# Kernel optimization log

Hardware: AMD Instinct MI355X
Metric: run time of the kernel (lower is better)

The kernel has to match this reference:

```python
import jax, jax.numpy as jnp
import numpy as np

B = 1024
HP_ORDER = 4
N_GRID = 72 * (8 ** HP_ORDER)  # 294912 rotations in the SO(3) healpix grid


def _random_rotmats(key, n):
    """Uniform random rotation matrices via normalized quaternions."""
    q = jax.random.normal(key, (n, 4), dtype=jnp.float32)
    q = q / jnp.linalg.norm(q, axis=-1, keepdims=True)
    w, x, y, z = q[:, 0], q[:, 1], q[:, 2], q[:, 3]
    R = jnp.stack([
        jnp.stack([1 - 2 * (y * y + z * z), 2 * (x * y - w * z), 2 * (x * z + w * y)], axis=-1),
        jnp.stack([2 * (x * y + w * z), 1 - 2 * (x * x + z * z), 2 * (y * z - w * x)], axis=-1),
        jnp.stack([2 * (x * z - w * y), 2 * (y * z + w * x), 1 - 2 * (x * x + y * y)], axis=-1),
    ], axis=-2)  # [n, 3, 3]
    return R


def setup_inputs() -> dict:
    key = jax.random.key(0)
    k1, k2 = jax.random.split(key)
    rotMat = _random_rotmats(k1, B)            # [B, 3, 3] query rotations
    output_rotmats = _random_rotmats(k2, N_GRID)  # [N, 3, 3] fixed grid (buffer)
    return {"rotMat": rotMat, "output_rotmats": output_rotmats}


def reference(rotMat, output_rotmats):
    # trace(A @ R_n^T) == sum_ij A_ij * R_n_ij  -> GEMM with K=9
    sim = jnp.einsum('bij,nij->bn', rotMat, output_rotmats)  # [B, N]
    idxs = jnp.argmax(sim, axis=1)                            # [B]
    dot_trace = jnp.max(sim, axis=1)                          # [B]
    nearest = output_rotmats[idxs]                            # [B, 3, 3]
    return dot_trace, nearest
```

## Files before the change

### kernel.cpp

```cpp
#include <hip/hip_runtime.h>

#define B_TOTAL 1024
#define NGRID   294912
#define NTILES  (NGRID / 16)
#define MARGIN  6e-4f
#define CAP     (1u << 20)

#define QBLK    256
#define QTILES  (QBLK / 16)
#define NSLICE  512
#define TPB     (NTILES / NSLICE)
#define TPW2    (TPB / 4)

#define KEYS_OFF   0u
#define WSMAX_OFF  8192u
#define CNT_OFF    12288u
#define CAND_OFF   16384u
#define APACK_OFF  4210688u
#define GPACK_OFF  4276224u
#define WS_NEED    23150592u

typedef __attribute__((ext_vector_type(8))) short short8v;
typedef __attribute__((ext_vector_type(4))) float float4v;

__device__ __forceinline__ unsigned short f2bf(float x) {
    unsigned u = __float_as_uint(x);
    unsigned r = ((u >> 16) & 1u) + 0x7FFFu;
    return (unsigned short)((u + r) >> 16);
}
__device__ __forceinline__ float bf2f(unsigned short b) {
    return __uint_as_float(((unsigned)b) << 16);
}
__device__ __forceinline__ unsigned ford(float f) {
    unsigned u = __float_as_uint(f);
    return (u & 0x80000000u) ? ~u : (u | 0x80000000u);
}
__device__ __forceinline__ float funord(unsigned u) {
    return __uint_as_float((u & 0x80000000u) ? (u & 0x7FFFFFFFu) : ~u);
}

__global__ __launch_bounds__(256)
void so3_init_kernel(unsigned long long* __restrict__ keys,
                     unsigned* __restrict__ wsmax, unsigned* __restrict__ cnt) {
    int i = blockIdx.x * 256 + threadIdx.x;
    if (i < B_TOTAL) { keys[i] = 0ull; wsmax[i] = 0u; }
    if (i == 0) *cnt = 0u;
}

__global__ __launch_bounds__(256)
void so3_pack_kernel(const float* __restrict__ src, unsigned* __restrict__ dst,
                     int nrows, int isA) {
    int id = blockIdx.x * 256 + threadIdx.x;
    if (id >= nrows * 16) return;
    int r = id >> 4, i = id & 15;
    unsigned w = 0;
    #pragma unroll
    for (int h = 0; h < 2; ++h) {
        int s = i * 2 + h;
        unsigned short v = 0;
        if (s < 27) {
            int k = (s < 9) ? s : (s < 18 ? s - 9 : s - 18);
            float x = src[(size_t)r * 9 + k];
            unsigned short hi = f2bf(x);
            int wantLo = isA ? (s >= 18) : (s >= 9 && s < 18);
            v = wantLo ? f2bf(x - bf2f(hi)) : hi;
        }
        w |= ((unsigned)v) << (16 * h);
    }
    dst[id] = w;
}

__device__ __forceinline__ void stage_A(const unsigned short* __restrict__ Ap,
                                        unsigned short* sB, int t, int qbase) {
    #pragma unroll
    for (int i = 0; i < QBLK / 64; ++i) {
        int id = t + i * 256;
        int row = id >> 2, kb = id & 3;
        uint4 v = *(const uint4*)(Ap + (size_t)(qbase + row) * 32 + kb * 8);
        int skb = kb ^ ((row >> 1) & 3);
        *(uint4*)((char*)sB + row * 64 + skb * 16) = v;
    }
}

__device__ __forceinline__ float tree_max9(const float* m4) {
    float a = fmaxf(fmaxf(m4[0], m4[1]), m4[2]);
    float b = fmaxf(fmaxf(m4[3], m4[4]), m4[5]);
    float c = fmaxf(fmaxf(m4[6], m4[7]), m4[8]);
    return fmaxf(fmaxf(a, b), c);
}

__global__ __launch_bounds__(256, 4)
void so3_mfma_max_kernel(const unsigned short* __restrict__ Ap,
                         const unsigned short* __restrict__ Gp,
                         unsigned* __restrict__ wsmax) {
    __shared__ __align__(16) unsigned short sB[QBLK * 32];
    __shared__ float sW[4][QTILES][4][16];
    const int t = threadIdx.x, l = t & 63, w = t >> 6;
    const int lr = l & 15, lk = l >> 4;
    const int qbase = blockIdx.y * QBLK;

    stage_A(Ap, sB, t, qbase);

    const int tile0 = blockIdx.x * TPB + w * TPW2;
    short8v af[TPW2];
    #pragma unroll
    for (int i = 0; i < TPW2; ++i)
        af[i] = *(const short8v*)(Gp + (size_t)((tile0 + i) * 16 + lr) * 32 + lk * 8);

    __syncthreads();

    for (int qt = 0; qt < QTILES; ++qt) {
        const int row = qt * 16 + lr;
        const int skb = lk ^ ((row >> 1) & 3);
        short8v bf = *(const short8v*)((const char*)sB + row * 64 + skb * 16);
        float m4[TPW2];
        #pragma unroll
        for (int i = 0; i < TPW2; ++i) {
            float4v c = {0.f, 0.f, 0.f, 0.f};
            c = __builtin_amdgcn_mfma_f32_16x16x32_bf16(af[i], bf, c, 0, 0, 0);
            m4[i] = fmaxf(fmaxf(c[0], c[1]), fmaxf(c[2], c[3]));
        }
        sW[w][qt][lk][lr] = tree_max9(m4);
    }
    __syncthreads();

    {
        int e = t;
        int qt = e >> 4, q = e & 15;
        float v = -1e30f;
        #pragma unroll
        for (int ww = 0; ww < 4; ++ww)
            #pragma unroll
            for (int kk = 0; kk < 4; ++kk)
                v = fmaxf(v, sW[ww][qt][kk][q]);
        unsigned u = ford(v);
        unsigned* p = wsmax + qbase + e;
        if (u > *p) atomicMax(p, u);
    }
}

__global__ __launch_bounds__(256, 4)
void so3_mfma_cand_kernel(const unsigned short* __restrict__ Ap,
                          const unsigned short* __restrict__ Gp,
                          const unsigned* __restrict__ wsmax,
                          unsigned* __restrict__ cnt,
                          unsigned* __restrict__ cands) {
    __shared__ __align__(16) unsigned short sB[QBLK * 32];
    __shared__ float sThr[QBLK];
    const int t = threadIdx.x, l = t & 63, w = t >> 6;
    const int lr = l & 15, lk = l >> 4;
    const int qbase = blockIdx.y * QBLK;

    stage_A(Ap, sB, t, qbase);
    sThr[t] = funord(wsmax[qbase + t]) - MARGIN;

    const int tile0 = blockIdx.x * TPB + w * TPW2;
    short8v af[TPW2];
    #pragma unroll
    for (int i = 0; i < TPW2; ++i)
        af[i] = *(const short8v*)(Gp + (size_t)((tile0 + i) * 16 + lr) * 32 + lk * 8);

    __syncthreads();

    for (int qt = 0; qt < QTILES; ++qt) {
        const int row = qt * 16 + lr;
        const float thr = sThr[row];
        const int skb = lk ^ ((row >> 1) & 3);
        short8v bf = *(const short8v*)((const char*)sB + row * 64 + skb * 16);
        #pragma unroll
        for (int i = 0; i < TPW2; ++i) {
            float4v c = {0.f, 0.f, 0.f, 0.f};
            c = __builtin_amdgcn_mfma_f32_16x16x32_bf16(af[i], bf, c, 0, 0, 0);
            float m4 = fmaxf(fmaxf(c[0], c[1]), fmaxf(c[2], c[3]));
            if (m4 >= thr) {
                int b = qbase + row;
                #pragma unroll
                for (int r = 0; r < 4; ++r) {
                    if (c[r] >= thr) {
                        int n = (tile0 + i) * 16 + lk * 4 + r;
                        unsigned idx = atomicAdd(cnt, 1u);
                        if (idx < CAP)
                            cands[idx] = ((unsigned)b << 19) | (unsigned)n;
                    }
                }
            }
        }
    }
}

__global__ __launch_bounds__(256)
void so3_rescore_kernel(const float* __restrict__ A, const float* __restrict__ G,
                        const unsigned* __restrict__ cnt,
                        const unsigned* __restrict__ cands,
                        unsigned long long* __restrict__ keys) {
    unsigned total = *cnt;
    if (total > CAP) total = CAP;
    const unsigned stride = gridDim.x * 256;
    for (unsigned i = blockIdx.x * 256 + threadIdx.x; i < total; i += stride) {
        unsigned cd = cands[i];
        int b = (int)(cd >> 19), n = (int)(cd & 0x7FFFFu);
        const float* a = A + (size_t)b * 9;
        const float* g = G + (size_t)n * 9;
        float d;
        d = a[0] * g[0];
        d = fmaf(a[1], g[1], d);
        d = fmaf(a[2], g[2], d);
        d = fmaf(a[3], g[3], d);
        d = fmaf(a[4], g[4], d);
        d = fmaf(a[5], g[5], d);
        d = fmaf(a[6], g[6], d);
        d = fmaf(a[7], g[7], d);
        d = fmaf(a[8], g[8], d);
        unsigned long long key =
            ((unsigned long long)ford(d) << 32) | (unsigned)(~n);
        unsigned long long seen = keys[b];
        if (key > seen) atomicMax(&keys[b], key);
    }
}

__global__ __launch_bounds__(256)
void so3_final_kernel(const float* __restrict__ G,
                      const unsigned long long* __restrict__ keys,
                      float* __restrict__ out) {
    int b = blockIdx.x * 256 + threadIdx.x;
    if (b >= B_TOTAL) return;
    unsigned long long key = keys[b];
    unsigned hi = (unsigned)(key >> 32);
    int idx = (int)(~(unsigned)key);
    out[b] = funord(hi);
    const float* g = G + (size_t)idx * 9;
    float* o = out + B_TOTAL + (size_t)b * 9;
    #pragma unroll
    for (int k = 0; k < 9; ++k) o[k] = g[k];
}

#define FB_NBLK  2048
#define FB_CHUNK (NGRID / FB_NBLK)
#define FB_NTHR  128
#define FB_BPT   8
__global__ __launch_bounds__(FB_NTHR, 4)
void so3_fb_partial_kernel(const float* __restrict__ A, const float* __restrict__ G,
                           unsigned long long* __restrict__ ws) {
    __shared__ __align__(16) float sG[FB_CHUNK * 12];
    const int t = threadIdx.x;
    const int n0 = blockIdx.x * FB_CHUNK;
    for (int i = t; i < FB_CHUNK * 9; i += FB_NTHR) {
        int row = i / 9, k = i - row * 9;
        sG[row * 12 + k] = G[(size_t)n0 * 9 + i];
    }
    float a[FB_BPT][9];
    #pragma unroll
    for (int j = 0; j < FB_BPT; ++j) {
        const float* ap = A + (size_t)(j * FB_NTHR + t) * 9;
        #pragma unroll
        for (int k = 0; k < 9; ++k) a[j][k] = ap[k];
    }
    float best[FB_BPT]; int bidx[FB_BPT];
    #pragma unroll
    for (int j = 0; j < FB_BPT; ++j) { best[j] = -1e30f; bidx[j] = 0; }
    __syncthreads();
    #pragma unroll 2
    for (int n = 0; n < FB_CHUNK; ++n) {
        const float4* gv = (const float4*)(sG + n * 12);
        const float4 gA = gv[0], gB = gv[1];
        const float g8 = sG[n * 12 + 8];
        const int vn = n0 + n;
        #pragma unroll
        for (int j = 0; j < FB_BPT; ++j) {
            float d;
            d = a[j][0] * gA.x; d = fmaf(a[j][1], gA.y, d); d = fmaf(a[j][2], gA.z, d);
            d = fmaf(a[j][3], gA.w, d); d = fmaf(a[j][4], gB.x, d); d = fmaf(a[j][5], gB.y, d);
            d = fmaf(a[j][6], gB.z, d); d = fmaf(a[j][7], gB.w, d); d = fmaf(a[j][8], g8, d);
            if (d > best[j]) { best[j] = d; bidx[j] = vn; }
        }
    }
    #pragma unroll
    for (int j = 0; j < FB_BPT; ++j) {
        unsigned long long key =
            ((unsigned long long)ford(best[j]) << 32) | (unsigned)(~bidx[j]);
        unsigned long long seen = ws[j * FB_NTHR + t];
        if (key > seen) atomicMax(&ws[j * FB_NTHR + t], key);
    }
}

extern "C" void kernel_launch(void* const* d_in, const int* in_sizes, int n_in,
                              void* d_out, int out_size, void* d_ws, size_t ws_size,
                              hipStream_t stream) {
    const float* A = (const float*)d_in[0];
    const float* G = (const float*)d_in[1];
    float* out = (float*)d_out;
    char* ws = (char*)d_ws;
    unsigned long long* keys = (unsigned long long*)(ws + KEYS_OFF);
    unsigned* wsmax = (unsigned*)(ws + WSMAX_OFF);
    unsigned* cnt   = (unsigned*)(ws + CNT_OFF);
    unsigned* cands = (unsigned*)(ws + CAND_OFF);
    unsigned short* Ap = (unsigned short*)(ws + APACK_OFF);
    unsigned short* Gp = (unsigned short*)(ws + GPACK_OFF);

    if (ws_size < WS_NEED) {
        hipLaunchKernelGGL(so3_init_kernel, dim3(4), dim3(256), 0, stream,
                           keys, wsmax, cnt);
        hipLaunchKernelGGL(so3_fb_partial_kernel, dim3(FB_NBLK), dim3(FB_NTHR),
                           0, stream, A, G, keys);
        hipLaunchKernelGGL(so3_final_kernel, dim3(4), dim3(256), 0, stream,
                           G, keys, out);
        return;
    }

    hipLaunchKernelGGL(so3_init_kernel, dim3(4), dim3(256), 0, stream,
                       keys, wsmax, cnt);
    hipLaunchKernelGGL(so3_pack_kernel, dim3((B_TOTAL * 16) / 256), dim3(256),
                       0, stream, A, (unsigned*)Ap, B_TOTAL, 1);
    hipLaunchKernelGGL(so3_pack_kernel, dim3((NGRID * 16) / 256), dim3(256),
                       0, stream, G, (unsigned*)Gp, NGRID, 0);
    hipLaunchKernelGGL(so3_mfma_max_kernel, dim3(NSLICE, B_TOTAL / QBLK),
                       dim3(256), 0, stream, Ap, Gp, wsmax);
    hipLaunchKernelGGL(so3_mfma_cand_kernel, dim3(NSLICE, B_TOTAL / QBLK),
                       dim3(256), 0, stream, Ap, Gp, wsmax, cnt, cands);
    hipLaunchKernelGGL(so3_rescore_kernel, dim3(128), dim3(256), 0, stream,
                       A, G, cnt, cands, keys);
    hipLaunchKernelGGL(so3_final_kernel, dim3(4), dim3(256), 0, stream,
                       G, keys, out);
}
```

Measured before the change: 87.90 us.

## Fuse max and candidate passes into one kernel with block-local threshold

Merges the max-reduction and candidate-collection kernels into a single kernel that computes a per-block query max, then filters candidates against that local threshold. Candidates are buffered in shared memory and flushed with one global atomic per block, and the slice count is halved so each wave handles more tiles. This removes a launch, the global max round-trip and per-candidate global atomics. The trade-off is that the local threshold is looser, so more candidates reach rescoring and the CAP overflow risk grows.

New measurement: 147.5 us. 67.7% more time.

```diff
diff --git a/kernel.cpp b/kernel.cpp
--- a/kernel.cpp
+++ b/kernel.cpp
@@ -8,12 +8,12 @@
 
 #define QBLK    256
 #define QTILES  (QBLK / 16)
-#define NSLICE  512
+#define NSLICE  256
 #define TPB     (NTILES / NSLICE)
-#define TPW2    (TPB / 4)
+#define TPW     (TPB / 4)
+#define SCAP    4096
 
 #define KEYS_OFF   0u
-#define WSMAX_OFF  8192u
 #define CNT_OFF    12288u
 #define CAND_OFF   16384u
 #define APACK_OFF  4210688u
@@ -41,9 +41,9 @@
 
 __global__ __launch_bounds__(256)
 void so3_init_kernel(unsigned long long* __restrict__ keys,
-                     unsigned* __restrict__ wsmax, unsigned* __restrict__ cnt) {
+                     unsigned* __restrict__ cnt) {
     int i = blockIdx.x * 256 + threadIdx.x;
-    if (i < B_TOTAL) { keys[i] = 0ull; wsmax[i] = 0u; }
+    if (i < B_TOTAL) keys[i] = 0ull;
     if (i == 0) *cnt = 0u;
 }
 
@@ -82,110 +82,98 @@
     }
 }
 
-__device__ __forceinline__ float tree_max9(const float* m4) {
-    float a = fmaxf(fmaxf(m4[0], m4[1]), m4[2]);
-    float b = fmaxf(fmaxf(m4[3], m4[4]), m4[5]);
-    float c = fmaxf(fmaxf(m4[6], m4[7]), m4[8]);
-    return fmaxf(fmaxf(a, b), c);
-}
-
 __global__ __launch_bounds__(256, 4)
-void so3_mfma_max_kernel(const unsigned short* __restrict__ Ap,
-                         const unsigned short* __restrict__ Gp,
-                         unsigned* __restrict__ wsmax) {
+void so3_fused_kernel(const unsigned short* __restrict__ Ap,
+                      const unsigned short* __restrict__ Gp,
+                      unsigned* __restrict__ cnt,
+                      unsigned* __restrict__ cands) {
     __shared__ __align__(16) unsigned short sB[QBLK * 32];
     __shared__ float sW[4][QTILES][4][16];
+    __shared__ float sThr[QBLK];
+    __shared__ unsigned sCand[SCAP];
+    __shared__ unsigned sCnt, sBase;
+
     const int t = threadIdx.x, l = t & 63, w = t >> 6;
     const int lr = l & 15, lk = l >> 4;
     const int qbase = blockIdx.y * QBLK;
 
     stage_A(Ap, sB, t, qbase);
-
-    const int tile0 = blockIdx.x * TPB + w * TPW2;
-    short8v af[TPW2];
-    #pragma unroll
-    for (int i = 0; i < TPW2; ++i)
+    if (t == 0) sCnt = 0;
+
+    const int tile0 = blockIdx.x * TPB + w * TPW;
+    short8v af[TPW];
+    #pragma unroll
+    for (int i = 0; i < TPW; ++i)
         af[i] = *(const short8v*)(Gp + (size_t)((tile0 + i) * 16 + lr) * 32 + lk * 8);
 
     __syncthreads();
 
+    #pragma unroll 2
     for (int qt = 0; qt < QTILES; ++qt) {
         const int row = qt * 16 + lr;
         const int skb = lk ^ ((row >> 1) & 3);
         short8v bf = *(const short8v*)((const char*)sB + row * 64 + skb * 16);
-        float m4[TPW2];
-        #pragma unroll
-        for (int i = 0; i < TPW2; ++i) {
+        float m = -1e30f;
+        #pragma unroll
+        for (int i = 0; i < TPW; ++i) {
             float4v c = {0.f, 0.f, 0.f, 0.f};
             c = __builtin_amdgcn_mfma_f32_16x16x32_bf16(af[i], bf, c, 0, 0, 0);
-            m4[i] = fmaxf(fmaxf(c[0], c[1]), fmaxf(c[2], c[3]));
+            float m3 = fmaxf(fmaxf(c[0], c[1]), c[2]);
+            m = fmaxf(fmaxf(m3, c[3]), m);
         }
-        sW[w][qt][lk][lr] = tree_max9(m4);
+        sW[w][qt][lk][lr] = m;
     }
     __syncthreads();
 
     {
-        int e = t;
-        int qt = e >> 4, q = e & 15;
+        int qt = t >> 4, q = t & 15;
         float v = -1e30f;
         #pragma unroll
         for (int ww = 0; ww < 4; ++ww)
             #pragma unroll
             for (int kk = 0; kk < 4; ++kk)
                 v = fmaxf(v, sW[ww][qt][kk][q]);
-        unsigned u = ford(v);
-        unsigned* p = wsmax + qbase + e;
-        if (u > *p) atomicMax(p, u);
-    }
-}
-
-__global__ __launch_bounds__(256, 4)
-void so3_mfma_cand_kernel(const unsigned short* __restrict__ Ap,
-                          const unsigned short* __restrict__ Gp,
-                          const unsigned* __restrict__ wsmax,
-                          unsigned* __restrict__ cnt,
-                          unsigned* __restrict__ cands) {
-    __shared__ __align__(16) unsigned short sB[QBLK * 32];
-    __shared__ float sThr[QBLK];
-    const int t = threadIdx.x, l = t & 63, w = t >> 6;
-    const int lr = l & 15, lk = l >> 4;
-    const int qbase = blockIdx.y * QBLK;
-
-    stage_A(Ap, sB, t, qbase);
-    sThr[t] = funord(wsmax[qbase + t]) - MARGIN;
-
-    const int tile0 = blockIdx.x * TPB + w * TPW2;
-    short8v af[TPW2];
-    #pragma unroll
-    for (int i = 0; i < TPW2; ++i)
-        af[i] = *(const short8v*)(Gp + (size_t)((tile0 + i) * 16 + lr) * 32 + lk * 8);
-
-    __syncthreads();
-
+        sThr[t] = v - MARGIN;
+    }
+    __syncthreads();
+
+    #pragma unroll 2
     for (int qt = 0; qt < QTILES; ++qt) {
         const int row = qt * 16 + lr;
         const float thr = sThr[row];
         const int skb = lk ^ ((row >> 1) & 3);
         short8v bf = *(const short8v*)((const char*)sB + row * 64 + skb * 16);
         #pragma unroll
-        for (int i = 0; i < TPW2; ++i) {
+        for (int i = 0; i < TPW; ++i) {
             float4v c = {0.f, 0.f, 0.f, 0.f};
             c = __builtin_amdgcn_mfma_f32_16x16x32_bf16(af[i], bf, c, 0, 0, 0);
-            float m4 = fmaxf(fmaxf(c[0], c[1]), fmaxf(c[2], c[3]));
+            float m4 = fmaxf(fmaxf(fmaxf(c[0], c[1]), c[2]), c[3]);
             if (m4 >= thr) {
-                int b = qbase + row;
+                unsigned b = (unsigned)(qbase + row);
                 #pragma unroll
                 for (int r = 0; r < 4; ++r) {
                     if (c[r] >= thr) {
-                        int n = (tile0 + i) * 16 + lk * 4 + r;
-                        unsigned idx = atomicAdd(cnt, 1u);
-                        if (idx < CAP)
-                            cands[idx] = ((unsigned)b << 19) | (unsigned)n;
+                        unsigned n = (unsigned)((tile0 + i) * 16 + lk * 4 + r);
+                        unsigned v = (b << 19) | n;
+                        unsigned idx = atomicAdd(&sCnt, 1u);
+                        if (idx < SCAP) sCand[idx] = v;
+                        else {
+                            unsigned gi = atomicAdd(cnt, 1u);
+                            if (gi < CAP) cands[gi] = v;
+                        }
                     }
                 }
             }
         }
     }
+    __syncthreads();
+
+    unsigned k = sCnt < SCAP ? sCnt : SCAP;
+    if (t == 0) sBase = atomicAdd(cnt, k);
+    __syncthreads();
+    unsigned base = sBase;
+    for (unsigned i = t; i < k; i += 256)
+        if (base + i < CAP) cands[base + i] = sCand[i];
 }
 
 __global__ __launch_bounds__(256)
@@ -291,7 +279,6 @@
     float* out = (float*)d_out;
     char* ws = (char*)d_ws;
     unsigned long long* keys = (unsigned long long*)(ws + KEYS_OFF);
-    unsigned* wsmax = (unsigned*)(ws + WSMAX_OFF);
     unsigned* cnt   = (unsigned*)(ws + CNT_OFF);
     unsigned* cands = (unsigned*)(ws + CAND_OFF);
     unsigned short* Ap = (unsigned short*)(ws + APACK_OFF);
@@ -299,7 +286,7 @@
 
     if (ws_size < WS_NEED) {
         hipLaunchKernelGGL(so3_init_kernel, dim3(4), dim3(256), 0, stream,
-                           keys, wsmax, cnt);
+                           keys, cnt);
         hipLaunchKernelGGL(so3_fb_partial_kernel, dim3(FB_NBLK), dim3(FB_NTHR),
                            0, stream, A, G, keys);
         hipLaunchKernelGGL(so3_final_kernel, dim3(4), dim3(256), 0, stream,
@@ -308,15 +295,13 @@
     }
 
     hipLaunchKernelGGL(so3_init_kernel, dim3(4), dim3(256), 0, stream,
-                       keys, wsmax, cnt);
+                       keys, cnt);
     hipLaunchKernelGGL(so3_pack_kernel, dim3((B_TOTAL * 16) / 256), dim3(256),
                        0, stream, A, (unsigned*)Ap, B_TOTAL, 1);
     hipLaunchKernelGGL(so3_pack_kernel, dim3((NGRID * 16) / 256), dim3(256),
                        0, stream, G, (unsigned*)Gp, NGRID, 0);
-    hipLaunchKernelGGL(so3_mfma_max_kernel, dim3(NSLICE, B_TOTAL / QBLK),
-                       dim3(256), 0, stream, Ap, Gp, wsmax);
-    hipLaunchKernelGGL(so3_mfma_cand_kernel, dim3(NSLICE, B_TOTAL / QBLK),
-                       dim3(256), 0, stream, Ap, Gp, wsmax, cnt, cands);
+    hipLaunchKernelGGL(so3_fused_kernel, dim3(NSLICE, B_TOTAL / QBLK),
+                       dim3(256), 0, stream, Ap, Gp, cnt, cands);
     hipLaunchKernelGGL(so3_rescore_kernel, dim3(128), dim3(256), 0, stream,
                        A, G, cnt, cands, keys);
     hipLaunchKernelGGL(so3_final_kernel, dim3(4), dim3(256), 0, stream,
```
